# Kernel optimization log

Measured on AMD Instinct MI355X. Metric: run time of the kernel, lower is better.

The kernel has to match this reference:

```python
import jax, jax.numpy as jnp
import numpy as np

EMBED_DIM = 1024
KEY_SIZE = 1024
VALUE_SIZE = 1024


def setup_inputs() -> dict:
    key = jax.random.key(0)
    k1, k2, k3, k4, k5 = jax.random.split(key, 5)
    B, L = 4, 4096
    s = 1.0 / np.sqrt(EMBED_DIM)
    return {
        "x": jax.random.normal(k1, (B, L, EMBED_DIM), dtype=jnp.float32),
        # torch nn.Linear weights: [out_features, in_features]
        "Wq": jax.random.normal(k2, (KEY_SIZE, EMBED_DIM), dtype=jnp.float32) * s,
        "Wk": jax.random.normal(k3, (KEY_SIZE, EMBED_DIM), dtype=jnp.float32) * s,
        "Wv": jax.random.normal(k4, (VALUE_SIZE, EMBED_DIM), dtype=jnp.float32) * s,
        "Wo": jax.random.normal(k5, (EMBED_DIM, VALUE_SIZE), dtype=jnp.float32) * s,
    }


def reference(x, Wq, Wk, Wv, Wo):
    # x: [B, L, E]
    q = jnp.einsum("ble,ke->blk", x, Wq)  # [B, L, K]
    k = jnp.einsum("ble,ke->blk", x, Wk)  # [B, L, K]
    v = jnp.einsum("ble,ve->blv", x, Wv)  # [B, L, V]
    K = k.shape[-1]
    # transposed (feature-axial) attention: att over feature dims, contracting seq L
    att = jnp.einsum("blk,blj->bkj", q, k) / jnp.sqrt(jnp.asarray(K, x.dtype))  # [B, K, K]
    att = jax.nn.softmax(att, axis=-1)
    # out[b,l,k] = sum_j att[b,k,j] * v[b,l,j]  (matmul(att, v^T) then transpose)
    out = jnp.einsum("bkj,blj->blk", att, v)  # [B, L, K]
    return jnp.einsum("blv,ev->ble", out, Wo)  # [B, L, E]
```

## Files before the change

kernel.cpp:

```cpp
#include <hip/hip_runtime.h>
#include <hip/hip_bf16.h>

typedef unsigned short u16;
typedef __bf16 bf16x8 __attribute__((ext_vector_type(8)));
typedef float f32x4 __attribute__((ext_vector_type(4)));

#define AS1 __attribute__((address_space(1)))
#define AS3 __attribute__((address_space(3)))

__device__ inline u16 f2bf(float f) {
  union { float f; unsigned int u; } c; c.f = f;
  unsigned int u = c.u;
  return (u16)((u + 0x7fffu + ((u >> 16) & 1u)) >> 16);
}

__global__ __launch_bounds__(256) void cvt_x_dual(const float* __restrict__ x,
                                                  u16* __restrict__ xbf,
                                                  u16* __restrict__ xT) {
  __shared__ u16 tile[64][68];
  const int t = threadIdx.x;
  const long e0 = (long)blockIdx.x * 64;
  const long l0 = (long)blockIdx.y * 64;
  const long b  = blockIdx.z;
  const int tr = t >> 4, tc = t & 15;
#pragma unroll
  for (int i = 0; i < 4; ++i) {
    const int r = tr + i * 16;
    const long gl = b * 4096 + l0 + r;
    float4 v = *reinterpret_cast<const float4*>(x + gl * 1024 + e0 + tc * 4);
    ushort4 o;
    o.x = f2bf(v.x); o.y = f2bf(v.y); o.z = f2bf(v.z); o.w = f2bf(v.w);
    *reinterpret_cast<ushort4*>(xbf + gl * 1024 + e0 + tc * 4) = o;
    *reinterpret_cast<ushort4*>(&tile[r][tc * 4]) = o;
  }
  __syncthreads();
#pragma unroll
  for (int i = 0; i < 4; ++i) {
    const int c = tr + i * 16;
    ushort4 o;
    o.x = tile[tc * 4 + 0][c]; o.y = tile[tc * 4 + 1][c];
    o.z = tile[tc * 4 + 2][c]; o.w = tile[tc * 4 + 3][c];
    *reinterpret_cast<ushort4*>(xT + b * (1024L * 4096) + (e0 + c) * 4096 + l0 + tc * 4) = o;
  }
}

__global__ __launch_bounds__(256) void cvt_w4(const float* __restrict__ a, const float* __restrict__ b,
                                              const float* __restrict__ c, const float* __restrict__ d,
                                              u16* __restrict__ oa, u16* __restrict__ ob,
                                              u16* __restrict__ oc, u16* __restrict__ od) {
  int i = blockIdx.x * 256 + threadIdx.x;
  const int which = i >> 18;
  const int j = i & 262143;
  const float* src = which == 0 ? a : which == 1 ? b : which == 2 ? c : d;
  u16* dst = which == 0 ? oa : which == 1 ? ob : which == 2 ? oc : od;
  float4 v = reinterpret_cast<const float4*>(src)[j];
  ushort4 o;
  o.x = f2bf(v.x); o.y = f2bf(v.y); o.z = f2bf(v.z); o.w = f2bf(v.w);
  reinterpret_cast<ushort4*>(dst)[j] = o;
}

__global__ __launch_bounds__(256) void transpose_bf16(
    const u16* __restrict__ src, long sLd, long sZ,
    u16* __restrict__ dst, long dLd, long dZ) {
  __shared__ u16 tile[64][68];
  const int t = threadIdx.x;
  const long r0 = (long)blockIdx.y * 64;
  const long c0 = (long)blockIdx.x * 64;
  const long z = blockIdx.z;
  const int tr = t >> 4, tc = t & 15;
#pragma unroll
  for (int i = 0; i < 4; ++i) {
    const int r = tr + i * 16;
    ushort4 v = *reinterpret_cast<const ushort4*>(src + z * sZ + (r0 + r) * sLd + c0 + tc * 4);
    *reinterpret_cast<ushort4*>(&tile[r][tc * 4]) = v;
  }
  __syncthreads();
#pragma unroll
  for (int i = 0; i < 4; ++i) {
    const int c = tr + i * 16;
    ushort4 o;
    o.x = tile[tc * 4 + 0][c]; o.y = tile[tc * 4 + 1][c];
    o.z = tile[tc * 4 + 2][c]; o.w = tile[tc * 4 + 3][c];
    *reinterpret_cast<ushort4*>(dst + z * dZ + (c0 + c) * dLd + r0 + tc * 4) = o;
  }
}

__device__ __forceinline__ void stage_half(const u16* __restrict__ g, long ld, int k0,
                                           u16* dst, int t) {
#pragma unroll
  for (int i = 0; i < 2; ++i) {
    const int c = i * 512 + t;
    const int r = c >> 3;
    const int s = c & 7;
    const int col = ((s ^ (r & 7)) << 3) + k0;
    __builtin_amdgcn_global_load_lds((const AS1 void*)(g + (long)r * ld + col),
                                     (AS3 void*)(dst + c * 8), 16, 0, 0);
  }
}

__device__ __forceinline__ bf16x8 frag_ld(const u16* s, int row, int colb) {
  return *reinterpret_cast<const bf16x8*>(
      reinterpret_cast<const char*>(s) + row * 128 + (colb ^ ((row & 7) << 4)));
}

#define BAR_PRE()       do { asm volatile("s_waitcnt vmcnt(6)" ::: "memory"); \
                             __builtin_amdgcn_s_barrier(); \
                             asm volatile("" ::: "memory"); } while (0)
#define BAR_POST()      do { asm volatile("" ::: "memory"); \
                             __builtin_amdgcn_s_barrier(); \
                             asm volatile("" ::: "memory"); } while (0)

template<bool OUT_F32>
__global__ __launch_bounds__(512, 2) void gemm_nt256(
    const u16* __restrict__ A, long lda, long sAz4, long sAz1,
    const u16* __restrict__ B, long ldb, long sBz4, long sBz1,
    void* __restrict__ Cv, long ldc, long sCz4, long sCz1,
    long cBatch, int cShift,
    int K, float scale)
{
  __shared__ u16 sm[2 * 32768] __attribute__((aligned(16)));

  const int t = threadIdx.x;
  int wg = blockIdx.x + gridDim.x * blockIdx.y;
  const int nwg = gridDim.x * gridDim.y;
  const int qq = nwg >> 3;
  wg = (wg & 7) * qq + (wg >> 3);
  const long m0 = (long)(wg % gridDim.x) * 256;
  const long n0 = (long)(wg / gridDim.x) * 256;
  const int z = blockIdx.z;
  const long azoff = (long)(z >> 2) * sAz4 + (long)(z & 3) * sAz1;
  const long bzoff = (long)(z >> 2) * sBz4 + (long)(z & 3) * sBz1;
  const u16* Ab = A + azoff + m0 * lda;
  const u16* Bb = B + bzoff + n0 * ldb;

  const int wid = t >> 6, lane = t & 63;
  const int lhi = lane >> 4, llo = lane & 15;
  const int wm = wid >> 2, wn = wid & 3;

  f32x4 acc[2][4][2][2] = {};
  const int NT = K >> 6;

  stage_half(Ab, lda, 0, sm, t);
  stage_half(Bb + 128 * ldb, ldb, 0, sm + 16384 + 8192, t);
  stage_half(Bb, ldb, 0, sm + 16384, t);
  stage_half(Ab + 128 * lda, lda, 0, sm + 8192, t);
  stage_half(Ab, lda, 64, sm + 32768, t);
  stage_half(Bb + 128 * ldb, ldb, 64, sm + 32768 + 16384 + 8192, t);
  asm volatile("s_waitcnt vmcnt(4)" ::: "memory");
  __builtin_amdgcn_s_barrier();
  asm volatile("" ::: "memory");

  for (int kt = 0; kt < NT; ++kt) {
    const int kb = kt & 1;
    u16* bc = sm + kb * 32768;
    u16* bn = sm + (kb ^ 1) * 32768;
    const u16* sAc = bc;
    const u16* sBc = bc + 16384;
    const int k1 = ((kt + 1 < NT) ? kt + 1 : 0) << 6;
    const int k2 = ((kt + 2 < NT) ? kt + 2 : kt + 2 - NT) << 6;

    bf16x8 a[4][2], bl[2][2], bh[2][2];

#pragma unroll
    for (int fr = 0; fr < 4; ++fr)
#pragma unroll
      for (int kk = 0; kk < 2; ++kk)
        a[fr][kk] = frag_ld(sAc, wm * 64 + fr * 16 + llo, (kk << 6) + (lhi << 4));
#pragma unroll
    for (int fc = 0; fc < 2; ++fc)
#pragma unroll
      for (int kk = 0; kk < 2; ++kk)
        bl[fc][kk] = frag_ld(sBc, wn * 32 + fc * 16 + llo, (kk << 6) + (lhi << 4));
    stage_half(Bb, ldb, k1, bn + 16384, t);
    BAR_PRE();
    __builtin_amdgcn_s_setprio(1);
#pragma unroll
    for (int fr = 0; fr < 4; ++fr)
#pragma unroll
      for (int fc = 0; fc < 2; ++fc)
#pragma unroll
        for (int kk = 0; kk < 2; ++kk)
          acc[0][fr][0][fc] = __builtin_amdgcn_mfma_f32_16x16x32_bf16(a[fr][kk], bl[fc][kk], acc[0][fr][0][fc], 0, 0, 0);
    __builtin_amdgcn_s_setprio(0);
    BAR_POST();

#pragma unroll
    for (int fc = 0; fc < 2; ++fc)
#pragma unroll
      for (int kk = 0; kk < 2; ++kk)
        bh[fc][kk] = frag_ld(sBc, 128 + wn * 32 + fc * 16 + llo, (kk << 6) + (lhi << 4));
    stage_half(Ab + 128 * lda, lda, k1, bn + 8192, t);
    BAR_PRE();
    __builtin_amdgcn_s_setprio(1);
#pragma unroll
    for (int fr = 0; fr < 4; ++fr)
#pragma unroll
      for (int fc = 0; fc < 2; ++fc)
#pragma unroll
        for (int kk = 0; kk < 2; ++kk)
          acc[0][fr][1][fc] = __builtin_amdgcn_mfma_f32_16x16x32_bf16(a[fr][kk], bh[fc][kk], acc[0][fr][1][fc], 0, 0, 0);
    __builtin_amdgcn_s_setprio(0);
    BAR_POST();

#pragma unroll
    for (int fr = 0; fr < 4; ++fr)
#pragma unroll
      for (int kk = 0; kk < 2; ++kk)
        a[fr][kk] = frag_ld(sAc, 128 + wm * 64 + fr * 16 + llo, (kk << 6) + (lhi << 4));
    stage_half(Ab, lda, k2, bc, t);
    BAR_PRE();
    __builtin_amdgcn_s_setprio(1);
#pragma unroll
    for (int fr = 0; fr < 4; ++fr)
#pragma unroll
      for (int fc = 0; fc < 2; ++fc)
#pragma unroll
        for (int kk = 0; kk < 2; ++kk)
          acc[1][fr][1][fc] = __builtin_amdgcn_mfma_f32_16x16x32_bf16(a[fr][kk], bh[fc][kk], acc[1][fr][1][fc], 0, 0, 0);
    __builtin_amdgcn_s_setprio(0);
    BAR_POST();

    stage_half(Bb + 128 * ldb, ldb, k2, bc + 16384 + 8192, t);
    BAR_PRE();
    __builtin_amdgcn_s_setprio(1);
#pragma unroll
    for (int fr = 0; fr < 4; ++fr)
#pragma unroll
      for (int fc = 0; fc < 2; ++fc)
#pragma unroll
        for (int kk = 0; kk < 2; ++kk)
          acc[1][fr][0][fc] = __builtin_amdgcn_mfma_f32_16x16x32_bf16(a[fr][kk], bl[fc][kk], acc[1][fr][0][fc], 0, 0, 0);
    __builtin_amdgcn_s_setprio(0);
    BAR_POST();
  }

  const long cb = n0 >> cShift;
  const long ncol0 = n0 - (cb << cShift);
  const long czoff = (long)(z >> 2) * sCz4 + (long)(z & 3) * sCz1 + cb * cBatch;
#pragma unroll
  for (int ah = 0; ah < 2; ++ah)
#pragma unroll
    for (int fr = 0; fr < 4; ++fr)
#pragma unroll
      for (int e = 0; e < 4; ++e) {
        const long r = m0 + ah * 128 + wm * 64 + fr * 16 + lhi * 4 + e;
#pragma unroll
        for (int bh2 = 0; bh2 < 2; ++bh2)
#pragma unroll
          for (int fc = 0; fc < 2; ++fc) {
            const long col = ncol0 + bh2 * 128 + wn * 32 + fc * 16 + llo;
            const float val = acc[ah][fr][bh2][fc][e] * scale;
            if (OUT_F32)
              ((float*)Cv)[czoff + r * ldc + col] = val;
            else
              ((u16*)Cv)[czoff + r * ldc + col] = f2bf(val);
          }
      }
}

__device__ __forceinline__ bf16x8 frag_ld128(const u16* s, int row, int lhi) {
  return *reinterpret_cast<const bf16x8*>(
      reinterpret_cast<const char*>(s) + row * 64 + ((lhi ^ (row & 3)) << 4));
}

template<bool OUT_F32>
__global__ __launch_bounds__(256) void gemm_nt128p(
    const u16* __restrict__ A, long lda, long sAz,
    const u16* __restrict__ B, long ldb, long sBz,
    void* __restrict__ Cv, long ldc, long sCz,
    int K, float scale)
{
  __shared__ u16 sm[3 * 8192] __attribute__((aligned(16)));

  const int t = threadIdx.x;
  int wg = blockIdx.x + gridDim.x * blockIdx.y;
  const int nwg = gridDim.x * gridDim.y;
  const int qq = nwg >> 3;
  wg = (wg & 7) * qq + (wg >> 3);
  const long m0 = (long)(wg % gridDim.x) * 128;
  const long n0 = (long)(wg / gridDim.x) * 128;
  const int z = blockIdx.z;
  A += (long)z * sAz + m0 * lda;
  B += (long)z * sBz + n0 * ldb;

  const int wid = t >> 6, lane = t & 63;
  const int lhi = lane >> 4, llo = lane & 15;
  const int wr = (wid >> 1) * 64, wc = (wid & 1) * 64;
  const int srow = t >> 2;
  const int scol = t & 3;

  f32x4 acc[4][4] = {};
  const int NT = K >> 5;

#define STAGE128(kk, buf)                                                              \
  do {                                                                                 \
    _Pragma("unroll")                                                                  \
    for (int c = 0; c < 2; ++c) {                                                      \
      const int row = c * 64 + srow;                                                   \
      const int col = ((scol ^ (row & 3)) << 3) + (kk);                                \
      __builtin_amdgcn_global_load_lds((const AS1 void*)(A + (long)row * lda + col),   \
                                       (AS3 void*)((buf) + (c * 256 + t) * 8), 16, 0, 0); \
      __builtin_amdgcn_global_load_lds((const AS1 void*)(B + (long)row * ldb + col),   \
                                       (AS3 void*)((buf) + 4096 + (c * 256 + t) * 8), 16, 0, 0); \
    }                                                                                  \
  } while (0)

  STAGE128(0, sm);
  STAGE128(32, sm + 8192);
  STAGE128(64, sm + 16384);

  for (int kt = 0; kt < NT; ++kt) {
    asm volatile("s_waitcnt vmcnt(8)" ::: "memory");
    __builtin_amdgcn_s_barrier();
    asm volatile("" ::: "memory");
    u16* buf = sm + (kt % 3) * 8192;
    const u16* sA = buf;
    const u16* sB = buf + 4096;
    bf16x8 af[4], bfr[4];
#pragma unroll
    for (int i = 0; i < 4; ++i) af[i] = frag_ld128(sA, wr + i * 16 + llo, lhi);
#pragma unroll
    for (int j = 0; j < 4; ++j) bfr[j] = frag_ld128(sB, wc + j * 16 + llo, lhi);
    __builtin_amdgcn_s_setprio(1);
#pragma unroll
    for (int i = 0; i < 4; ++i)
#pragma unroll
      for (int j = 0; j < 4; ++j)
        acc[i][j] = __builtin_amdgcn_mfma_f32_16x16x32_bf16(af[i], bfr[j], acc[i][j], 0, 0, 0);
    __builtin_amdgcn_s_setprio(0);
    asm volatile("" ::: "memory");
    __builtin_amdgcn_s_barrier();
    asm volatile("" ::: "memory");
    const int k3 = ((kt + 3 < NT) ? kt + 3 : kt + 3 - NT) << 5;
    STAGE128(k3, buf);
  }

#pragma unroll
  for (int i = 0; i < 4; ++i) {
#pragma unroll
    for (int e = 0; e < 4; ++e) {
      const long r = m0 + wr + i * 16 + lhi * 4 + e;
      if (OUT_F32) {
        float* C = (float*)Cv + (long)z * sCz + r * ldc + n0 + wc + llo;
#pragma unroll
        for (int j = 0; j < 4; ++j) C[j * 16] = acc[i][j][e] * scale;
      } else {
        u16* C = (u16*)Cv + (long)z * sCz + r * ldc + n0 + wc + llo;
#pragma unroll
        for (int j = 0; j < 4; ++j) C[j * 16] = f2bf(acc[i][j][e] * scale);
      }
    }
  }
}

__global__ __launch_bounds__(256) void greduce4(const float* __restrict__ gp,
                                                u16* __restrict__ gb) {
  const long i = (long)blockIdx.x * 256 + threadIdx.x;
  const long b = i >> 18;
  const long r = i & 262143;
  float4 s; s.x = 0.f; s.y = 0.f; s.z = 0.f; s.w = 0.f;
#pragma unroll
  for (int p = 0; p < 4; ++p) {
    const float4 u = reinterpret_cast<const float4*>(gp)[((b * 4 + p) << 18) + r];
    s.x += u.x; s.y += u.y; s.z += u.z; s.w += u.w;
  }
  ushort4 o;
  o.x = f2bf(s.x); o.y = f2bf(s.y); o.z = f2bf(s.z); o.w = f2bf(s.w);
  reinterpret_cast<ushort4*>(gb)[(b << 18) + r] = o;
}

__global__ __launch_bounds__(256) void softmax1(const float* __restrict__ att,
                                                u16* __restrict__ P) {
  const long row = blockIdx.x;
  const int t = threadIdx.x;
  float4 v = reinterpret_cast<const float4*>(att + row * 1024)[t];
  float m = fmaxf(fmaxf(v.x, v.y), fmaxf(v.z, v.w));
#pragma unroll
  for (int off = 32; off > 0; off >>= 1) m = fmaxf(m, __shfl_down(m, off, 64));
  __shared__ float smax[4], ssum[4];
  const int wid = t >> 6, lane = t & 63;
  if (lane == 0) smax[wid] = m;
  __syncthreads();
  m = fmaxf(fmaxf(smax[0], smax[1]), fmaxf(smax[2], smax[3]));
  float e0 = expf(v.x - m), e1 = expf(v.y - m), e2 = expf(v.z - m), e3 = expf(v.w - m);
  float s = e0 + e1 + e2 + e3;
#pragma unroll
  for (int off = 32; off > 0; off >>= 1) s += __shfl_down(s, off, 64);
  if (lane == 0) ssum[wid] = s;
  __syncthreads();
  s = ssum[0] + ssum[1] + ssum[2] + ssum[3];
  float inv = 1.0f / s;
  ushort4 o;
  o.x = f2bf(e0 * inv); o.y = f2bf(e1 * inv); o.z = f2bf(e2 * inv); o.w = f2bf(e3 * inv);
  reinterpret_cast<ushort4*>(P + row * 1024)[t] = o;
}

extern "C" void kernel_launch(void* const* d_in, const int* in_sizes, int n_in,
                              void* d_out, int out_size, void* d_ws, size_t ws_size,
                              hipStream_t stream) {
  const float* x  = (const float*)d_in[0];
  const float* Wq = (const float*)d_in[1];
  const float* Wk = (const float*)d_in[2];
  const float* Wv = (const float*)d_in[3];
  const float* Wo = (const float*)d_in[4];

  const long M1 = 1L << 20;

  u16* xbf  = (u16*)d_ws;
  u16* wq   = xbf + 16 * M1;
  u16* wk   = wq + M1;
  u16* wv   = wk + M1;
  u16* wo   = wv + M1;
  u16* wvT  = wo + M1;
  u16* xT   = wvT + M1;
  u16* gbf  = xT + 16 * M1;
  u16* tbuf = gbf + 4 * M1;
  u16* pbuf = tbuf + 4 * M1;
  u16* rtb  = pbuf + 4 * M1;
  u16* sbuf = rtb + 4 * M1;
  float* gpart = (float*)d_out;
  float* attf  = (float*)d_out;

  dim3 b256(256), b512(512);
  const long NOF = 0;
  const int NSH = 30;

  cvt_x_dual<<<dim3(16, 64, 4), b256, 0, stream>>>(x, xbf, xT);
  cvt_w4<<<dim3(4096), b256, 0, stream>>>(Wq, Wk, Wv, Wo, wq, wk, wv, wo);
  transpose_bf16<<<dim3(16, 16, 1), b256, 0, stream>>>(wv, 1024, 0, wvT, 1024, 0);

  gemm_nt256<true><<<dim3(4, 4, 16), b512, 0, stream>>>(
      xT, 4096, 1024L * 4096, 1024, xT, 4096, 1024L * 4096, 1024,
      (void*)gpart, 1024, 4L << 20, 1L << 20, NOF, NSH, 1024, 1.0f);
  greduce4<<<dim3(4096), b256, 0, stream>>>(gpart, gbf);

  gemm_nt128p<false><<<dim3(8, 8, 4), b256, 0, stream>>>(
      wq, 1024, 0, gbf, 1024, M1, (void*)tbuf, 1024, M1, 1024, 1.0f);
  gemm_nt128p<true><<<dim3(8, 8, 4), b256, 0, stream>>>(
      tbuf, 1024, M1, wk, 1024, 0, (void*)attf, 1024, M1, 1024, 1.0f / 32.0f);
  softmax1<<<dim3(4096), b256, 0, stream>>>(attf, pbuf);

  gemm_nt128p<false><<<dim3(8, 8, 4), b256, 0, stream>>>(
      wvT, 1024, 0, pbuf, 1024, M1, (void*)rtb, 1024, M1, 1024, 1.0f);
  gemm_nt128p<false><<<dim3(8, 8, 4), b256, 0, stream>>>(
      wo, 1024, 0, rtb, 1024, M1, (void*)sbuf, 1024, M1, 1024, 1.0f);

  gemm_nt256<true><<<dim3(16, 4, 4), b512, 0, stream>>>(
      xbf, 1024, 0, 4096L * 1024, sbuf, 1024, 0, M1,
      d_out, 1024, 0, 4096L * 1024, NOF, NSH, 1024, 1.0f);
}
```

Baseline: 220.3 us.

## Widen small GEMMs to 8 waves and store Gram partials as bf16

The 128x128-tile GEMM now uses 512 threads (8 waves, each 64x32), with one staging load per thread per operand. This gives more waves per tile to hide latency on the 256-workgroup small GEMMs. Separately, the split-K Gram partials are written as bf16 to a workspace buffer instead of fp32, which halves the partial-sum traffic in the reduce kernel. In exchange, the partials are rounded to bf16 before they are summed, which costs some accuracy.

```diff
diff --git a/kernel.cpp b/kernel.cpp
--- a/kernel.cpp
+++ b/kernel.cpp
@@ -4,6 +4,7 @@
 typedef unsigned short u16;
 typedef __bf16 bf16x8 __attribute__((ext_vector_type(8)));
 typedef float f32x4 __attribute__((ext_vector_type(4)));
+typedef unsigned short ushort8 __attribute__((ext_vector_type(8)));
 
 #define AS1 __attribute__((address_space(1)))
 #define AS3 __attribute__((address_space(3)))
@@ -12,6 +13,10 @@
   union { float f; unsigned int u; } c; c.f = f;
   unsigned int u = c.u;
   return (u16)((u + 0x7fffu + ((u >> 16) & 1u)) >> 16);
+}
+__device__ inline float bf2f(u16 v) {
+  union { unsigned int u; float f; } c; c.u = ((unsigned int)v) << 16;
+  return c.f;
 }
 
 __global__ __launch_bounds__(256) void cvt_x_dual(const float* __restrict__ x,
@@ -264,7 +269,7 @@
 }
 
 template<bool OUT_F32>
-__global__ __launch_bounds__(256) void gemm_nt128p(
+__global__ __launch_bounds__(512, 2) void gemm_nt128w(
     const u16* __restrict__ A, long lda, long sAz,
     const u16* __restrict__ B, long ldb, long sBz,
     void* __restrict__ Cv, long ldc, long sCz,
@@ -285,54 +290,48 @@
 
   const int wid = t >> 6, lane = t & 63;
   const int lhi = lane >> 4, llo = lane & 15;
-  const int wr = (wid >> 1) * 64, wc = (wid & 1) * 64;
+  const int wr = (wid >> 2) * 64, wc = (wid & 3) * 32;
   const int srow = t >> 2;
   const int scol = t & 3;
 
-  f32x4 acc[4][4] = {};
+  f32x4 acc[4][2] = {};
   const int NT = K >> 5;
 
-#define STAGE128(kk, buf)                                                              \
-  do {                                                                                 \
-    _Pragma("unroll")                                                                  \
-    for (int c = 0; c < 2; ++c) {                                                      \
-      const int row = c * 64 + srow;                                                   \
-      const int col = ((scol ^ (row & 3)) << 3) + (kk);                                \
-      __builtin_amdgcn_global_load_lds((const AS1 void*)(A + (long)row * lda + col),   \
-                                       (AS3 void*)((buf) + (c * 256 + t) * 8), 16, 0, 0); \
-      __builtin_amdgcn_global_load_lds((const AS1 void*)(B + (long)row * ldb + col),   \
-                                       (AS3 void*)((buf) + 4096 + (c * 256 + t) * 8), 16, 0, 0); \
-    }                                                                                  \
+#define STAGEW(kk, buf)                                                                 \
+  do {                                                                                  \
+    const int col = ((scol ^ (srow & 3)) << 3) + (kk);                                  \
+    __builtin_amdgcn_global_load_lds((const AS1 void*)(A + (long)srow * lda + col),     \
+                                     (AS3 void*)((buf) + t * 8), 16, 0, 0);             \
+    __builtin_amdgcn_global_load_lds((const AS1 void*)(B + (long)srow * ldb + col),     \
+                                     (AS3 void*)((buf) + 4096 + t * 8), 16, 0, 0);      \
   } while (0)
 
-  STAGE128(0, sm);
-  STAGE128(32, sm + 8192);
-  STAGE128(64, sm + 16384);
+  STAGEW(0, sm);
+  STAGEW(32, sm + 8192);
+  STAGEW(64, sm + 16384);
 
   for (int kt = 0; kt < NT; ++kt) {
-    asm volatile("s_waitcnt vmcnt(8)" ::: "memory");
+    asm volatile("s_waitcnt vmcnt(4)" ::: "memory");
     __builtin_amdgcn_s_barrier();
     asm volatile("" ::: "memory");
     u16* buf = sm + (kt % 3) * 8192;
-    const u16* sA = buf;
-    const u16* sB = buf + 4096;
-    bf16x8 af[4], bfr[4];
-#pragma unroll
-    for (int i = 0; i < 4; ++i) af[i] = frag_ld128(sA, wr + i * 16 + llo, lhi);
-#pragma unroll
-    for (int j = 0; j < 4; ++j) bfr[j] = frag_ld128(sB, wc + j * 16 + llo, lhi);
+    bf16x8 af[4], bfr[2];
+#pragma unroll
+    for (int i = 0; i < 4; ++i) af[i] = frag_ld128(buf, wr + i * 16 + llo, lhi);
+#pragma unroll
+    for (int j = 0; j < 2; ++j) bfr[j] = frag_ld128(buf + 4096, wc + j * 16 + llo, lhi);
     __builtin_amdgcn_s_setprio(1);
 #pragma unroll
     for (int i = 0; i < 4; ++i)
 #pragma unroll
-      for (int j = 0; j < 4; ++j)
+      for (int j = 0; j < 2; ++j)
         acc[i][j] = __builtin_amdgcn_mfma_f32_16x16x32_bf16(af[i], bfr[j], acc[i][j], 0, 0, 0);
     __builtin_amdgcn_s_setprio(0);
     asm volatile("" ::: "memory");
     __builtin_amdgcn_s_barrier();
     asm volatile("" ::: "memory");
     const int k3 = ((kt + 3 < NT) ? kt + 3 : kt + 3 - NT) << 5;
-    STAGE128(k3, buf);
+    STAGEW(k3, buf);
   }
 
 #pragma unroll
@@ -343,30 +342,32 @@
       if (OUT_F32) {
         float* C = (float*)Cv + (long)z * sCz + r * ldc + n0 + wc + llo;
 #pragma unroll
-        for (int j = 0; j < 4; ++j) C[j * 16] = acc[i][j][e] * scale;
+        for (int j = 0; j < 2; ++j) C[j * 16] = acc[i][j][e] * scale;
       } else {
         u16* C = (u16*)Cv + (long)z * sCz + r * ldc + n0 + wc + llo;
 #pragma unroll
-        for (int j = 0; j < 4; ++j) C[j * 16] = f2bf(acc[i][j][e] * scale);
+        for (int j = 0; j < 2; ++j) C[j * 16] = f2bf(acc[i][j][e] * scale);
       }
     }
   }
 }
 
-__global__ __launch_bounds__(256) void greduce4(const float* __restrict__ gp,
-                                                u16* __restrict__ gb) {
-  const long i = (long)blockIdx.x * 256 + threadIdx.x;
-  const long b = i >> 18;
-  const long r = i & 262143;
-  float4 s; s.x = 0.f; s.y = 0.f; s.z = 0.f; s.w = 0.f;
+__global__ __launch_bounds__(256) void greduce4b(const u16* __restrict__ gp,
+                                                 u16* __restrict__ gb) {
+  const long o = (long)blockIdx.x * 256 + threadIdx.x;
+  const long b = o >> 17;
+  const long r = o & 131071;
+  float s[8] = {};
 #pragma unroll
   for (int p = 0; p < 4; ++p) {
-    const float4 u = reinterpret_cast<const float4*>(gp)[((b * 4 + p) << 18) + r];
-    s.x += u.x; s.y += u.y; s.z += u.z; s.w += u.w;
-  }
-  ushort4 o;
-  o.x = f2bf(s.x); o.y = f2bf(s.y); o.z = f2bf(s.z); o.w = f2bf(s.w);
-  reinterpret_cast<ushort4*>(gb)[(b << 18) + r] = o;
+    ushort8 u = reinterpret_cast<const ushort8*>(gp)[((b * 4 + p) << 17) + r];
+#pragma unroll
+    for (int j = 0; j < 8; ++j) s[j] += bf2f(u[j]);
+  }
+  ushort8 out;
+#pragma unroll
+  for (int j = 0; j < 8; ++j) out[j] = f2bf(s[j]);
+  reinterpret_cast<ushort8*>(gb)[o] = out;
 }
 
 __global__ __launch_bounds__(256) void softmax1(const float* __restrict__ att,
@@ -406,20 +407,20 @@
 
   const long M1 = 1L << 20;
 
-  u16* xbf  = (u16*)d_ws;
-  u16* wq   = xbf + 16 * M1;
-  u16* wk   = wq + M1;
-  u16* wv   = wk + M1;
-  u16* wo   = wv + M1;
-  u16* wvT  = wo + M1;
-  u16* xT   = wvT + M1;
-  u16* gbf  = xT + 16 * M1;
-  u16* tbuf = gbf + 4 * M1;
-  u16* pbuf = tbuf + 4 * M1;
-  u16* rtb  = pbuf + 4 * M1;
-  u16* sbuf = rtb + 4 * M1;
-  float* gpart = (float*)d_out;
-  float* attf  = (float*)d_out;
+  u16* xbf    = (u16*)d_ws;
+  u16* wq     = xbf + 16 * M1;
+  u16* wk     = wq + M1;
+  u16* wv     = wk + M1;
+  u16* wo     = wv + M1;
+  u16* wvT    = wo + M1;
+  u16* xT     = wvT + M1;
+  u16* gbf    = xT + 16 * M1;
+  u16* tbuf   = gbf + 4 * M1;
+  u16* pbuf   = tbuf + 4 * M1;
+  u16* rtb    = pbuf + 4 * M1;
+  u16* sbuf   = rtb + 4 * M1;
+  u16* gpartb = sbuf + 4 * M1;
+  float* attf = (float*)d_out;
 
   dim3 b256(256), b512(512);
   const long NOF = 0;
@@ -429,20 +430,20 @@
   cvt_w4<<<dim3(4096), b256, 0, stream>>>(Wq, Wk, Wv, Wo, wq, wk, wv, wo);
   transpose_bf16<<<dim3(16, 16, 1), b256, 0, stream>>>(wv, 1024, 0, wvT, 1024, 0);
 
-  gemm_nt256<true><<<dim3(4, 4, 16), b512, 0, stream>>>(
+  gemm_nt256<false><<<dim3(4, 4, 16), b512, 0, stream>>>(
       xT, 4096, 1024L * 4096, 1024, xT, 4096, 1024L * 4096, 1024,
-      (void*)gpart, 1024, 4L << 20, 1L << 20, NOF, NSH, 1024, 1.0f);
-  greduce4<<<dim3(4096), b256, 0, stream>>>(gpart, gbf);
-
-  gemm_nt128p<false><<<dim3(8, 8, 4), b256, 0, stream>>>(
+      (void*)gpartb, 1024, 4L << 20, 1L << 20, NOF, NSH, 1024, 1.0f);
+  greduce4b<<<dim3(2048), b256, 0, stream>>>(gpartb, gbf);
+
+  gemm_nt128w<false><<<dim3(8, 8, 4), b512, 0, stream>>>(
       wq, 1024, 0, gbf, 1024, M1, (void*)tbuf, 1024, M1, 1024, 1.0f);
-  gemm_nt128p<true><<<dim3(8, 8, 4), b256, 0, stream>>>(
+  gemm_nt128w<true><<<dim3(8, 8, 4), b512, 0, stream>>>(
       tbuf, 1024, M1, wk, 1024, 0, (void*)attf, 1024, M1, 1024, 1.0f / 32.0f);
   softmax1<<<dim3(4096), b256, 0, stream>>>(attf, pbuf);
 
-  gemm_nt128p<false><<<dim3(8, 8, 4), b256, 0, stream>>>(
+  gemm_nt128w<false><<<dim3(8, 8, 4), b512, 0, stream>>>(
       wvT, 1024, 0, pbuf, 1024, M1, (void*)rtb, 1024, M1, 1024, 1.0f);
-  gemm_nt128p<false><<<dim3(8, 8, 4), b256, 0, stream>>>(
+  gemm_nt128w<false><<<dim3(8, 8, 4), b512, 0, stream>>>(
       wo, 1024, 0, rtb, 1024, M1, (void*)sbuf, 1024, M1, 1024, 1.0f);
 
   gemm_nt256<true><<<dim3(16, 4, 4), b512, 0, stream>>>(
```

Result: faster. 197.3 us (-10.4%).
